# Optimization experiments

Measured on AMD Instinct MI355X. Metric: run time of the kernel, lower is better.

The kernel has to match this reference:

```python
import jax, jax.numpy as jnp
import numpy as np

B, S, D, H = 8, 1024, 1024, 16
DK = D // H


def setup_inputs() -> dict:
    key = jax.random.key(0)
    ks = jax.random.split(key, 10)
    scale = 1.0 / np.sqrt(D)
    return {
        "x": jax.random.normal(ks[0], (B, S, D), dtype=jnp.float32),
        "prefix": jax.random.randint(ks[1], (B,), 0, S, dtype=jnp.int32),
        "Wq": jax.random.normal(ks[2], (D, D), dtype=jnp.float32) * scale,
        "bq": jnp.zeros((D,), dtype=jnp.float32),
        "Wk": jax.random.normal(ks[3], (D, D), dtype=jnp.float32) * scale,
        "bk": jnp.zeros((D,), dtype=jnp.float32),
        "Wv": jax.random.normal(ks[4], (D, D), dtype=jnp.float32) * scale,
        "bv": jnp.zeros((D,), dtype=jnp.float32),
        "Wo": jax.random.normal(ks[5], (D, D), dtype=jnp.float32) * scale,
        "bo": jnp.zeros((D,), dtype=jnp.float32),
    }


def reference(x, prefix, Wq, bq, Wk, bk, Wv, bv, Wo, bo):
    b, s, d = x.shape
    h, dk = H, DK
    # projections -> [b, h, s, dk]
    def split_heads(t):
        return t.reshape(b, s, h, dk).transpose(0, 2, 1, 3)
    q = split_heads(x @ Wq + bq)
    k = split_heads(x @ Wk + bk)
    v = split_heads(x @ Wv + bv)
    # raw scores (no 1/sqrt(dk) scaling in the original)
    scores = jnp.einsum('bhqd,bhkd->bhqk', q, k)
    # mask construction (faithful to original, incl. final permute/transpose):
    # allowed[b, q, k] = (q < prefix[b]) or (k >= q)
    q_idx = jnp.arange(s)[:, None]   # [s, 1]
    k_idx = jnp.arange(s)[None, :]   # [1, s]
    allowed = (q_idx[None, :, :] < prefix[:, None, None]) | (k_idx >= q_idx)  # [b, s, s]
    scores = jnp.where(allowed[:, None, :, :], scores, -jnp.inf)
    probs = jax.nn.softmax(scores, axis=-1)
    # einsum -> bqhd, then transpose(1,2) -> bhqd, then view(b, s, d) (faithful
    # to the original's head-interleaving reshape)
    out = jnp.einsum('bhql,bhld->bqhd', probs, v)
    out = out.transpose(0, 2, 1, 3).reshape(b, s, d)
    return out @ Wo + bo
```

## Files before the change

### kernel.cpp

```cpp
#include <hip/hip_runtime.h>
#include <stdint.h>

typedef __attribute__((ext_vector_type(8)))  short          short8;
typedef __attribute__((ext_vector_type(8)))  unsigned short u16x8;
typedef __attribute__((ext_vector_type(4)))  unsigned short u16x4;
typedef __attribute__((ext_vector_type(4)))  float          f32x4;
typedef __attribute__((ext_vector_type(16))) float          f32x16;

__device__ __forceinline__ unsigned short f2bf(float x) {
  unsigned int u = __float_as_uint(x);
  u += 0x7fffu + ((u >> 16) & 1u);
  return (unsigned short)(u >> 16);
}
__device__ __forceinline__ float bf2f(unsigned short b) {
  return __uint_as_float(((unsigned int)b) << 16);
}

__device__ __forceinline__ void mfma16(f32x4& c, short8 a, short8 b) {
  asm volatile("v_mfma_f32_16x16x32_bf16 %0, %1, %2, %0" : "+v"(c) : "v"(a), "v"(b));
}
__device__ __forceinline__ void mfma32(f32x16& c, short8 a, short8 b) {
  asm volatile("v_mfma_f32_32x32x16_bf16 %0, %1, %2, %0" : "+v"(c) : "v"(a), "v"(b));
}
__device__ __forceinline__ float hw_exp2(float x) {
  float r;
  asm("v_exp_f32 %0, %1" : "=v"(r) : "v"(x));
  return r;
}

#define GLDS(gsrc, ldst)                                                    \
  __builtin_amdgcn_global_load_lds(                                         \
      (const __attribute__((address_space(1))) void*)(gsrc),                \
      (__attribute__((address_space(3))) void*)(ldst), 16, 0, 0)

__global__ void split_x_kernel(const float4* __restrict__ x,
                               ushort4* __restrict__ xh, int n4) {
  int stride = gridDim.x * blockDim.x;
  for (int i = blockIdx.x * blockDim.x + threadIdx.x; i < n4; i += stride) {
    float4 v = x[i];
    ushort4 h;
    h.x = f2bf(v.x);
    h.y = f2bf(v.y);
    h.z = f2bf(v.z);
    h.w = f2bf(v.w);
    xh[i] = h;
  }
}

__global__ void wsplit_kernel(const float* __restrict__ Wq, const float* __restrict__ Wk,
                              const float* __restrict__ Wv, const float* __restrict__ Wo,
                              unsigned short* qkv, unsigned short* oh) {
  __shared__ float tile[32][33];
  int z = blockIdx.z;
  const float* W = (z == 0) ? Wq : (z == 1) ? Wk : (z == 2) ? Wv : Wo;
  unsigned short* Oh = (z < 3) ? qkv + (size_t)z * 1024 * 1024 : oh;
  int k0 = blockIdx.y * 32, n0 = blockIdx.x * 32;
  int tx = threadIdx.x & 31, ty = threadIdx.x >> 5;
#pragma unroll
  for (int j = 0; j < 4; ++j)
    tile[ty + 8 * j][tx] = W[(size_t)(k0 + ty + 8 * j) * 1024 + n0 + tx];
  __syncthreads();
#pragma unroll
  for (int j = 0; j < 4; ++j) {
    float v = tile[tx][ty + 8 * j];
    size_t idx = (size_t)(n0 + ty + 8 * j) * 1024 + k0 + tx;
    Oh[idx] = f2bf(v);
  }
}

__global__ __launch_bounds__(256)
void qkv_gemm_kernel(const unsigned short* __restrict__ Ah,
                     const unsigned short* __restrict__ Bh,
                     const float* __restrict__ bq, const float* __restrict__ bk,
                     const float* __restrict__ bv,
                     unsigned short* __restrict__ QK, unsigned short* __restrict__ VT) {
  __shared__ unsigned short smem[128 * 136];
  unsigned short* sAh = smem;
  unsigned short* sBh = smem + 8192;
  const int K = 1024, M = 8192;

  int t = threadIdx.x;
  int wid = t >> 6, l = t & 63;
  int wm = wid >> 1, wn = wid & 1;
  int bm = blockIdx.y * 128, bn = blockIdx.x * 128;

  f32x4 acc[4][4] = {};

  for (int k0 = 0; k0 < K; k0 += 64) {
#pragma unroll
    for (int r = 0; r < 4; ++r) {
      int o = (r * 256 + t) << 4;
      int row = o >> 7;
      int gce = ((o & 127) ^ ((row & 7) << 4)) >> 1;
      int wb  = (o & ~1023) >> 1;
      size_t gA = (size_t)(bm + row) * K + k0 + gce;
      size_t gB = (size_t)(bn + row) * K + k0 + gce;
      GLDS(Ah + gA, sAh + wb);
      GLDS(Bh + gB, sBh + wb);
    }
    __syncthreads();
#pragma unroll
    for (int kh = 0; kh < 2; ++kh) {
      short8 afh[4], bfh[4];
#pragma unroll
      for (int m = 0; m < 4; ++m) {
        int row = wm * 64 + m * 16 + (l & 15);
        int cb = (((l >> 4) * 16 + kh * 64) ^ ((row & 7) << 4)) >> 1;
        afh[m] = *(const short8*)(sAh + row * 64 + cb);
      }
#pragma unroll
      for (int n = 0; n < 4; ++n) {
        int row = wn * 64 + n * 16 + (l & 15);
        int cb = (((l >> 4) * 16 + kh * 64) ^ ((row & 7) << 4)) >> 1;
        bfh[n] = *(const short8*)(sBh + row * 64 + cb);
      }
#pragma unroll
      for (int m = 0; m < 4; ++m)
#pragma unroll
        for (int n = 0; n < 4; ++n)
          mfma16(acc[m][n], afh[m], bfh[n]);
    }
    __syncthreads();
  }

  if (bn >= 2048) {
    int vb = bn - 2048;
    unsigned short* sT = smem;
#pragma unroll
    for (int m = 0; m < 4; ++m) {
      int lrow0 = wm * 64 + m * 16 + (l >> 4) * 4;
#pragma unroll
      for (int n = 0; n < 4; ++n) {
        int lcol = wn * 64 + n * 16 + (l & 15);
        float bs = bv[vb + lcol];
        u16x4 w;
#pragma unroll
        for (int r = 0; r < 4; ++r) w[r] = f2bf(acc[m][n][r] + bs);
        *(u16x4*)&sT[lcol * 136 + lrow0] = w;
      }
    }
    __syncthreads();
#pragma unroll
    for (int j = 0; j < 8; ++j) {
      int c = (t >> 4) + 16 * j;
      int r = (t & 15) * 8;
      *(u16x8*)(VT + (size_t)(vb + c) * M + bm + r) = *(const u16x8*)&sT[c * 136 + r];
    }
    return;
  }

#pragma unroll
  for (int m = 0; m < 4; ++m) {
    int grow0 = bm + wm * 64 + m * 16 + (l >> 4) * 4;
#pragma unroll
    for (int n = 0; n < 4; ++n) {
      int gcol = bn + wn * 64 + n * 16 + (l & 15);
      float bs = (gcol < 1024) ? bq[gcol] : bk[gcol - 1024];
#pragma unroll
      for (int r = 0; r < 4; ++r)
        QK[(size_t)(grow0 + r) * 2048 + gcol] = f2bf(acc[m][n][r] + bs);
    }
  }
}

__global__ __launch_bounds__(256)
void gemm_out_kernel(const unsigned short* __restrict__ Ah,
                     const unsigned short* __restrict__ Bh,
                     const float* __restrict__ bias, float* __restrict__ Cf,
                     int M, int N, int K) {
  __shared__ unsigned short smem[2 * 8192];
  unsigned short* sAh = smem;
  unsigned short* sBh = smem + 8192;

  int t = threadIdx.x;
  int wid = t >> 6, l = t & 63;
  int wm = wid >> 1, wn = wid & 1;
  int bm = blockIdx.y * 128, bn = blockIdx.x * 128;

  f32x4 acc[4][4] = {};

  for (int k0 = 0; k0 < K; k0 += 64) {
#pragma unroll
    for (int r = 0; r < 4; ++r) {
      int o = (r * 256 + t) << 4;
      int row = o >> 7;
      int gce = ((o & 127) ^ ((row & 7) << 4)) >> 1;
      int wb  = (o & ~1023) >> 1;
      size_t gA = (size_t)(bm + row) * K + k0 + gce;
      size_t gB = (size_t)(bn + row) * K + k0 + gce;
      GLDS(Ah + gA, sAh + wb);
      GLDS(Bh + gB, sBh + wb);
    }
    __syncthreads();
#pragma unroll
    for (int kh = 0; kh < 2; ++kh) {
      short8 afh[4], bfh[4];
#pragma unroll
      for (int m = 0; m < 4; ++m) {
        int row = wm * 64 + m * 16 + (l & 15);
        int cb = (((l >> 4) * 16 + kh * 64) ^ ((row & 7) << 4)) >> 1;
        afh[m] = *(const short8*)(sAh + row * 64 + cb);
      }
#pragma unroll
      for (int n = 0; n < 4; ++n) {
        int row = wn * 64 + n * 16 + (l & 15);
        int cb = (((l >> 4) * 16 + kh * 64) ^ ((row & 7) << 4)) >> 1;
        bfh[n] = *(const short8*)(sBh + row * 64 + cb);
      }
#pragma unroll
      for (int m = 0; m < 4; ++m)
#pragma unroll
        for (int n = 0; n < 4; ++n)
          mfma16(acc[m][n], afh[m], bfh[n]);
    }
    __syncthreads();
  }
#pragma unroll
  for (int m = 0; m < 4; ++m) {
    int grow0 = bm + wm * 64 + m * 16 + (l >> 4) * 4;
#pragma unroll
    for (int n = 0; n < 4; ++n) {
      int gcol = bn + wn * 64 + n * 16 + (l & 15);
      float bs = bias[gcol];
#pragma unroll
      for (int r = 0; r < 4; ++r)
        Cf[(size_t)(grow0 + r) * N + gcol] = acc[m][n][r] + bs;
    }
  }
}

__global__ __launch_bounds__(128)
void attn_kernel(const unsigned short* __restrict__ QK,
                 const unsigned short* __restrict__ VT, const int* __restrict__ prefix,
                 unsigned short* __restrict__ AOh) {
  const float NEG = -3.0e38f;
  const float L2E = 1.4426950408889634f;
  const float MC  = 46.16624410f;
  __shared__ unsigned short sKh[2][32][66];
  __shared__ unsigned short sV [2][64][34];

  int bh = blockIdx.x;
  int b = bh >> 4, h = bh & 15;
  int t = threadIdx.x, wid = t >> 6, l = t & 63;
  int qb0 = blockIdx.y * 64;
  int qb = qb0 + wid * 32;
  int P = prefix[b];
  int lq = l & 31, g = l >> 5;
  int q = qb + lq;
  bool qfull = (q < P);
  bool allfull = (P >= qb + 32);

  short8 bqh[4];
  {
    size_t base = (size_t)(b * 1024 + q) * 2048 + h * 64 + g * 8;
#pragma unroll
    for (int c = 0; c < 4; ++c)
      bqh[c] = *(const short8*)(QK + base + c * 16);
  }

  const unsigned short* KhB = QK + (size_t)b * 1024 * 2048 + 1024 + h * 64;
  const unsigned short* VTB = VT + (size_t)(h * 64) * 8192 + b * 1024;

  int srow = t >> 3, scol = (t & 7) * 8;
  int vrow = t >> 2, vcol = (t & 3) * 8;

  int kt0 = (qb0 >= P) ? qb0 : 0;
  int ntiles = (1024 - kt0) >> 5;

  f32x16 o0 = {}, o1 = {};
  float lrun = 0.f;

  int cur = 0;
  auto body = [&](int kt) {
    bool wave_dead = (qb >= P) && (kt + 31 < qb);
    if (wave_dead) return;
    f32x16 s = {};
    __builtin_amdgcn_s_setprio(1);
#pragma unroll
    for (int c = 0; c < 4; ++c) {
      short8 ah = *(const short8*)&sKh[cur][lq][g * 8 + c * 16];
      mfma32(s, ah, bqh[c]);
    }
    __builtin_amdgcn_s_setprio(0);

    float p[16];
    if (allfull || kt > qb) {
#pragma unroll
      for (int r = 0; r < 16; ++r)
        p[r] = hw_exp2(__builtin_fmaf(s[r], L2E, -MC));
    } else {
#pragma unroll
      for (int r = 0; r < 16; ++r) {
        int k = kt + (r & 3) + 8 * (r >> 2) + 4 * g;
        float sv = (qfull || k >= q) ? s[r] : NEG;
        p[r] = hw_exp2(__builtin_fmaf(sv, L2E, -MC));
      }
    }
    float s01 = p[0] + p[1],  s23 = p[2] + p[3],  s45 = p[4] + p[5],  s67 = p[6] + p[7];
    float s89 = p[8] + p[9],  sab = p[10] + p[11], scd = p[12] + p[13], sef = p[14] + p[15];
    lrun += ((s01 + s23) + (s45 + s67)) + ((s89 + sab) + (scd + sef));

    unsigned int w0, w1, w2, w3, w4, w5, w6, w7;
    asm("v_cvt_pk_bf16_f32 %0, %1, %2" : "=v"(w0) : "v"(p[0]),  "v"(p[1]));
    asm("v_cvt_pk_bf16_f32 %0, %1, %2" : "=v"(w1) : "v"(p[2]),  "v"(p[3]));
    asm("v_cvt_pk_bf16_f32 %0, %1, %2" : "=v"(w2) : "v"(p[4]),  "v"(p[5]));
    asm("v_cvt_pk_bf16_f32 %0, %1, %2" : "=v"(w3) : "v"(p[6]),  "v"(p[7]));
    asm("v_cvt_pk_bf16_f32 %0, %1, %2" : "=v"(w4) : "v"(p[8]),  "v"(p[9]));
    asm("v_cvt_pk_bf16_f32 %0, %1, %2" : "=v"(w5) : "v"(p[10]), "v"(p[11]));
    asm("v_cvt_pk_bf16_f32 %0, %1, %2" : "=v"(w6) : "v"(p[12]), "v"(p[13]));
    asm("v_cvt_pk_bf16_f32 %0, %1, %2" : "=v"(w7) : "v"(p[14]), "v"(p[15]));
    {
      unsigned int v0 = g ? w0 : w2, r0 = __shfl_xor(v0, 32);
      unsigned int v1 = g ? w1 : w3, r1 = __shfl_xor(v1, 32);
      unsigned int v4 = g ? w4 : w6, r4 = __shfl_xor(v4, 32);
      unsigned int v5 = g ? w5 : w7, r5 = __shfl_xor(v5, 32);
      unsigned int n0 = g ? r0 : w0, n2 = g ? w2 : r0;
      unsigned int n1 = g ? r1 : w1, n3 = g ? w3 : r1;
      unsigned int n4 = g ? r4 : w4, n6 = g ? w6 : r4;
      unsigned int n5 = g ? r5 : w5, n7 = g ? w7 : r5;
      w0 = n0; w1 = n1; w2 = n2; w3 = n3; w4 = n4; w5 = n5; w6 = n6; w7 = n7;
    }
    union { unsigned int u[4]; short8 v; } B0, B1;
    B0.u[0] = w0; B0.u[1] = w1; B0.u[2] = w2; B0.u[3] = w3;
    B1.u[0] = w4; B1.u[1] = w5; B1.u[2] = w6; B1.u[3] = w7;

    short8 va00 = *(const short8*)&sV[cur][lq][g * 8];
    short8 va01 = *(const short8*)&sV[cur][lq][16 + g * 8];
    short8 va10 = *(const short8*)&sV[cur][32 + lq][g * 8];
    short8 va11 = *(const short8*)&sV[cur][32 + lq][16 + g * 8];
    __builtin_amdgcn_s_setprio(1);
    mfma32(o0, va00, B0.v);
    mfma32(o0, va01, B1.v);
    mfma32(o1, va10, B0.v);
    mfma32(o1, va11, B1.v);
    __builtin_amdgcn_s_setprio(0);
  };

  u16x8 akh0, akh1, av0, av1;
  u16x8 bkh0, bkh1, bv0, bv1;
  akh0 = *(const u16x8*)(KhB + (size_t)(kt0 + srow) * 2048 + scol);
  akh1 = *(const u16x8*)(KhB + (size_t)(kt0 + srow + 16) * 2048 + scol);
  av0  = *(const u16x8*)(VTB + (size_t)vrow * 8192 + kt0 + vcol);
  av1  = *(const u16x8*)(VTB + (size_t)(vrow + 32) * 8192 + kt0 + vcol);
  *(u16x8*)&sKh[0][srow][scol]      = akh0;
  *(u16x8*)&sKh[0][srow + 16][scol] = akh1;
  *(u16x8*)&sV [0][vrow][vcol]      = av0;
  *(u16x8*)&sV [0][vrow + 32][vcol] = av1;
  {
    int kt1 = kt0 + ((1 < ntiles) ? 32 : 0);
    akh0 = *(const u16x8*)(KhB + (size_t)(kt1 + srow) * 2048 + scol);
    akh1 = *(const u16x8*)(KhB + (size_t)(kt1 + srow + 16) * 2048 + scol);
    av0  = *(const u16x8*)(VTB + (size_t)vrow * 8192 + kt1 + vcol);
    av1  = *(const u16x8*)(VTB + (size_t)(vrow + 32) * 8192 + kt1 + vcol);
  }
  __syncthreads();

  int i = 0;
  while (true) {
    {
      int i2 = (i + 2 < ntiles) ? (i + 2) : (ntiles - 1);
      int kt2 = kt0 + i2 * 32;
      bkh0 = *(const u16x8*)(KhB + (size_t)(kt2 + srow) * 2048 + scol);
      bkh1 = *(const u16x8*)(KhB + (size_t)(kt2 + srow + 16) * 2048 + scol);
      bv0  = *(const u16x8*)(VTB + (size_t)vrow * 8192 + kt2 + vcol);
      bv1  = *(const u16x8*)(VTB + (size_t)(vrow + 32) * 8192 + kt2 + vcol);
      body(kt0 + i * 32);
      if (i + 1 < ntiles) {
        *(u16x8*)&sKh[cur ^ 1][srow][scol]      = akh0;
        *(u16x8*)&sKh[cur ^ 1][srow + 16][scol] = akh1;
        *(u16x8*)&sV [cur ^ 1][vrow][vcol]      = av0;
        *(u16x8*)&sV [cur ^ 1][vrow + 32][vcol] = av1;
      }
      __syncthreads();
      cur ^= 1; ++i;
      if (i >= ntiles) break;
    }
    {
      int i2 = (i + 2 < ntiles) ? (i + 2) : (ntiles - 1);
      int kt2 = kt0 + i2 * 32;
      akh0 = *(const u16x8*)(KhB + (size_t)(kt2 + srow) * 2048 + scol);
      akh1 = *(const u16x8*)(KhB + (size_t)(kt2 + srow + 16) * 2048 + scol);
      av0  = *(const u16x8*)(VTB + (size_t)vrow * 8192 + kt2 + vcol);
      av1  = *(const u16x8*)(VTB + (size_t)(vrow + 32) * 8192 + kt2 + vcol);
      body(kt0 + i * 32);
      if (i + 1 < ntiles) {
        *(u16x8*)&sKh[cur ^ 1][srow][scol]      = bkh0;
        *(u16x8*)&sKh[cur ^ 1][srow + 16][scol] = bkh1;
        *(u16x8*)&sV [cur ^ 1][vrow][vcol]      = bv0;
        *(u16x8*)&sV [cur ^ 1][vrow + 32][vcol] = bv1;
      }
      __syncthreads();
      cur ^= 1; ++i;
      if (i >= ntiles) break;
    }
  }

  lrun += __shfl_xor(lrun, 32);

  float inv = 1.0f / lrun;
  size_t obase = (size_t)(b * 1024 + h * 64 + (q >> 4)) * 1024 + (q & 15) * 64;
#pragma unroll
  for (int tt = 0; tt < 4; ++tt) {
    u16x4 w0, w1;
#pragma unroll
    for (int j = 0; j < 4; ++j) {
      w0[j] = f2bf(o0[4 * tt + j] * inv);
      w1[j] = f2bf(o1[4 * tt + j] * inv);
    }
    *(u16x4*)(AOh + obase + 8 * tt + 4 * g)      = w0;
    *(u16x4*)(AOh + obase + 32 + 8 * tt + 4 * g) = w1;
  }
}

extern "C" void kernel_launch(void* const* d_in, const int* in_sizes, int n_in,
                              void* d_out, int out_size, void* d_ws, size_t ws_size,
                              hipStream_t stream) {
  (void)in_sizes; (void)n_in; (void)out_size;
  const float* x      = (const float*)d_in[0];
  const int*   prefix = (const int*)d_in[1];
  const float* Wq = (const float*)d_in[2];
  const float* bq = (const float*)d_in[3];
  const float* Wk = (const float*)d_in[4];
  const float* bk = (const float*)d_in[5];
  const float* Wv = (const float*)d_in[6];
  const float* bv = (const float*)d_in[7];
  const float* Wo = (const float*)d_in[8];
  const float* bo = (const float*)d_in[9];
  float* out = (float*)d_out;

  const size_t MBY = 1ull << 20;
  if (ws_size < 144 * MBY) return;
  char* ws = (char*)d_ws;
  unsigned short* xh   = (unsigned short*)(ws + 0 * MBY);
  unsigned short* wqkv = (unsigned short*)(ws + 32 * MBY);
  unsigned short* woh  = (unsigned short*)(ws + 44 * MBY);
  unsigned short* QK   = (unsigned short*)(ws + 48 * MBY);
  unsigned short* AOh  = (unsigned short*)(ws + 112 * MBY);
  unsigned short* VT   = (unsigned short*)(ws + 128 * MBY);

  split_x_kernel<<<1024, 256, 0, stream>>>((const float4*)x, (ushort4*)xh, 8192 * 1024 / 4);
  wsplit_kernel<<<dim3(32, 32, 4), 256, 0, stream>>>(Wq, Wk, Wv, Wo, wqkv, woh);
  qkv_gemm_kernel<<<dim3(24, 64), 256, 0, stream>>>(xh, wqkv, bq, bk, bv, QK, VT);
  attn_kernel<<<dim3(128, 16), 128, 0, stream>>>(QK, VT, prefix, AOh);
  gemm_out_kernel<<<dim3(8, 64), 256, 0, stream>>>(AOh, woh, bo, out, 8192, 1024, 1024);
}
```

Before: 166.5 us.

## Load attention K/V tiles directly into registers with single-wave blocks

The attention kernel drops the shared-memory K/V staging and its barriers. Each single-wave block now loads its K and V MFMA fragments straight from global memory into registers, double-buffered two tiles ahead, and the grid doubles to match. K/V tiles are no longer shared between two waves, so global/L2 traffic per query block roughly doubles. The per-wave dead-tile skip is also gone, so each block now starts directly at its own start tile.

```diff
diff --git a/kernel.cpp b/kernel.cpp
--- a/kernel.cpp
+++ b/kernel.cpp
@@ -11,9 +11,6 @@
   unsigned int u = __float_as_uint(x);
   u += 0x7fffu + ((u >> 16) & 1u);
   return (unsigned short)(u >> 16);
-}
-__device__ __forceinline__ float bf2f(unsigned short b) {
-  return __uint_as_float(((unsigned int)b) << 16);
 }
 
 __device__ __forceinline__ void mfma16(f32x4& c, short8 a, short8 b) {
@@ -229,23 +226,20 @@
   }
 }
 
-__global__ __launch_bounds__(128)
+__global__ __launch_bounds__(64)
 void attn_kernel(const unsigned short* __restrict__ QK,
                  const unsigned short* __restrict__ VT, const int* __restrict__ prefix,
                  unsigned short* __restrict__ AOh) {
   const float NEG = -3.0e38f;
   const float L2E = 1.4426950408889634f;
   const float MC  = 46.16624410f;
-  __shared__ unsigned short sKh[2][32][66];
-  __shared__ unsigned short sV [2][64][34];
 
   int bh = blockIdx.x;
   int b = bh >> 4, h = bh & 15;
-  int t = threadIdx.x, wid = t >> 6, l = t & 63;
-  int qb0 = blockIdx.y * 64;
-  int qb = qb0 + wid * 32;
+  int l = threadIdx.x;
+  int lq = l & 31, g = l >> 5;
+  int qb = blockIdx.y * 32;
   int P = prefix[b];
-  int lq = l & 31, g = l >> 5;
   int q = qb + lq;
   bool qfull = (q < P);
   bool allfull = (P >= qb + 32);
@@ -258,29 +252,34 @@
       bqh[c] = *(const short8*)(QK + base + c * 16);
   }
 
-  const unsigned short* KhB = QK + (size_t)b * 1024 * 2048 + 1024 + h * 64;
-  const unsigned short* VTB = VT + (size_t)(h * 64) * 8192 + b * 1024;
-
-  int srow = t >> 3, scol = (t & 7) * 8;
-  int vrow = t >> 2, vcol = (t & 3) * 8;
-
-  int kt0 = (qb0 >= P) ? qb0 : 0;
+  const unsigned short* KhB = QK + (size_t)b * 1024 * 2048 + 1024 + h * 64 + g * 8;
+  const unsigned short* VTB = VT + (size_t)(h * 64 + lq) * 8192 + b * 1024 + g * 8;
+
+  int kt0 = (qb >= P) ? qb : 0;
   int ntiles = (1024 - kt0) >> 5;
 
   f32x16 o0 = {}, o1 = {};
   float lrun = 0.f;
 
-  int cur = 0;
-  auto body = [&](int kt) {
-    bool wave_dead = (qb >= P) && (kt + 31 < qb);
-    if (wave_dead) return;
+  auto loadK = [&](int kt, short8* kf) {
+    size_t rb = (size_t)(kt + lq) * 2048;
+#pragma unroll
+    for (int c = 0; c < 4; ++c)
+      kf[c] = *(const short8*)(KhB + rb + c * 16);
+  };
+  auto loadV = [&](int kt, short8* vf) {
+    vf[0] = *(const short8*)(VTB + kt);
+    vf[1] = *(const short8*)(VTB + kt + 16);
+    vf[2] = *(const short8*)(VTB + (size_t)32 * 8192 + kt);
+    vf[3] = *(const short8*)(VTB + (size_t)32 * 8192 + kt + 16);
+  };
+
+  auto body = [&](int kt, const short8* kf, const short8* vf) {
     f32x16 s = {};
     __builtin_amdgcn_s_setprio(1);
 #pragma unroll
-    for (int c = 0; c < 4; ++c) {
-      short8 ah = *(const short8*)&sKh[cur][lq][g * 8 + c * 16];
-      mfma32(s, ah, bqh[c]);
-    }
+    for (int c = 0; c < 4; ++c)
+      mfma32(s, kf[c], bqh[c]);
     __builtin_amdgcn_s_setprio(0);
 
     float p[16];
@@ -324,74 +323,40 @@
     B0.u[0] = w0; B0.u[1] = w1; B0.u[2] = w2; B0.u[3] = w3;
     B1.u[0] = w4; B1.u[1] = w5; B1.u[2] = w6; B1.u[3] = w7;
 
-    short8 va00 = *(const short8*)&sV[cur][lq][g * 8];
-    short8 va01 = *(const short8*)&sV[cur][lq][16 + g * 8];
-    short8 va10 = *(const short8*)&sV[cur][32 + lq][g * 8];
-    short8 va11 = *(const short8*)&sV[cur][32 + lq][16 + g * 8];
     __builtin_amdgcn_s_setprio(1);
-    mfma32(o0, va00, B0.v);
-    mfma32(o0, va01, B1.v);
-    mfma32(o1, va10, B0.v);
-    mfma32(o1, va11, B1.v);
+    mfma32(o0, vf[0], B0.v);
+    mfma32(o0, vf[1], B1.v);
+    mfma32(o1, vf[2], B0.v);
+    mfma32(o1, vf[3], B1.v);
     __builtin_amdgcn_s_setprio(0);
   };
 
-  u16x8 akh0, akh1, av0, av1;
-  u16x8 bkh0, bkh1, bv0, bv1;
-  akh0 = *(const u16x8*)(KhB + (size_t)(kt0 + srow) * 2048 + scol);
-  akh1 = *(const u16x8*)(KhB + (size_t)(kt0 + srow + 16) * 2048 + scol);
-  av0  = *(const u16x8*)(VTB + (size_t)vrow * 8192 + kt0 + vcol);
-  av1  = *(const u16x8*)(VTB + (size_t)(vrow + 32) * 8192 + kt0 + vcol);
-  *(u16x8*)&sKh[0][srow][scol]      = akh0;
-  *(u16x8*)&sKh[0][srow + 16][scol] = akh1;
-  *(u16x8*)&sV [0][vrow][vcol]      = av0;
-  *(u16x8*)&sV [0][vrow + 32][vcol] = av1;
+  short8 kA[4], vA[4], kB[4], vB[4];
+  loadK(kt0, kA);
+  loadV(kt0, vA);
   {
-    int kt1 = kt0 + ((1 < ntiles) ? 32 : 0);
-    akh0 = *(const u16x8*)(KhB + (size_t)(kt1 + srow) * 2048 + scol);
-    akh1 = *(const u16x8*)(KhB + (size_t)(kt1 + srow + 16) * 2048 + scol);
-    av0  = *(const u16x8*)(VTB + (size_t)vrow * 8192 + kt1 + vcol);
-    av1  = *(const u16x8*)(VTB + (size_t)(vrow + 32) * 8192 + kt1 + vcol);
-  }
-  __syncthreads();
+    int kt1 = kt0 + ((ntiles > 1) ? 32 : 0);
+    loadK(kt1, kB);
+    loadV(kt1, vB);
+  }
 
   int i = 0;
   while (true) {
     {
-      int i2 = (i + 2 < ntiles) ? (i + 2) : (ntiles - 1);
-      int kt2 = kt0 + i2 * 32;
-      bkh0 = *(const u16x8*)(KhB + (size_t)(kt2 + srow) * 2048 + scol);
-      bkh1 = *(const u16x8*)(KhB + (size_t)(kt2 + srow + 16) * 2048 + scol);
-      bv0  = *(const u16x8*)(VTB + (size_t)vrow * 8192 + kt2 + vcol);
-      bv1  = *(const u16x8*)(VTB + (size_t)(vrow + 32) * 8192 + kt2 + vcol);
-      body(kt0 + i * 32);
-      if (i + 1 < ntiles) {
-        *(u16x8*)&sKh[cur ^ 1][srow][scol]      = akh0;
-        *(u16x8*)&sKh[cur ^ 1][srow + 16][scol] = akh1;
-        *(u16x8*)&sV [cur ^ 1][vrow][vcol]      = av0;
-        *(u16x8*)&sV [cur ^ 1][vrow + 32][vcol] = av1;
-      }
-      __syncthreads();
-      cur ^= 1; ++i;
-      if (i >= ntiles) break;
+      body(kt0 + i * 32, kA, vA);
+      if (i + 2 < ntiles) {
+        loadK(kt0 + (i + 2) * 32, kA);
+        loadV(kt0 + (i + 2) * 32, vA);
+      }
+      ++i; if (i >= ntiles) break;
     }
     {
-      int i2 = (i + 2 < ntiles) ? (i + 2) : (ntiles - 1);
-      int kt2 = kt0 + i2 * 32;
-      akh0 = *(const u16x8*)(KhB + (size_t)(kt2 + srow) * 2048 + scol);
-      akh1 = *(const u16x8*)(KhB + (size_t)(kt2 + srow + 16) * 2048 + scol);
-      av0  = *(const u16x8*)(VTB + (size_t)vrow * 8192 + kt2 + vcol);
-      av1  = *(const u16x8*)(VTB + (size_t)(vrow + 32) * 8192 + kt2 + vcol);
-      body(kt0 + i * 32);
-      if (i + 1 < ntiles) {
-        *(u16x8*)&sKh[cur ^ 1][srow][scol]      = bkh0;
-        *(u16x8*)&sKh[cur ^ 1][srow + 16][scol] = bkh1;
-        *(u16x8*)&sV [cur ^ 1][vrow][vcol]      = bv0;
-        *(u16x8*)&sV [cur ^ 1][vrow + 32][vcol] = bv1;
-      }
-      __syncthreads();
-      cur ^= 1; ++i;
-      if (i >= ntiles) break;
+      body(kt0 + i * 32, kB, vB);
+      if (i + 2 < ntiles) {
+        loadK(kt0 + (i + 2) * 32, kB);
+        loadV(kt0 + (i + 2) * 32, vB);
+      }
+      ++i; if (i >= ntiles) break;
     }
   }
 
@@ -441,6 +406,6 @@
   split_x_kernel<<<1024, 256, 0, stream>>>((const float4*)x, (ushort4*)xh, 8192 * 1024 / 4);
   wsplit_kernel<<<dim3(32, 32, 4), 256, 0, stream>>>(Wq, Wk, Wv, Wo, wqkv, woh);
   qkv_gemm_kernel<<<dim3(24, 64), 256, 0, stream>>>(xh, wqkv, bq, bk, bv, QK, VT);
-  attn_kernel<<<dim3(128, 16), 128, 0, stream>>>(QK, VT, prefix, AOh);
+  attn_kernel<<<dim3(128, 32), 64, 0, stream>>>(QK, VT, prefix, AOh);
   gemm_out_kernel<<<dim3(8, 64), 256, 0, stream>>>(AOh, woh, bo, out, 8192, 1024, 1024);
 }
```

Result: slower. 207.3 us (+24.5%).

## Software-pipeline QK^T with softmax/PV in attention and merge prep kernels

Applied to the files above, without the earlier changes.

The attention loop is restructured so the QK^T MFMAs for tile i are issued before the softmax and PV work of tile i-1. This overlaps matrix-core work with exp and conversion ALU work, at the cost of an extra barrier per iteration and another live score accumulator. Separately, the x-to-bf16 conversion and the weight transpose/convert kernels are merged into one launch to cut launch overhead. The extra barrier and register pressure could reduce the benefit.

```diff
diff --git a/kernel.cpp b/kernel.cpp
--- a/kernel.cpp
+++ b/kernel.cpp
@@ -12,9 +12,6 @@
   u += 0x7fffu + ((u >> 16) & 1u);
   return (unsigned short)(u >> 16);
 }
-__device__ __forceinline__ float bf2f(unsigned short b) {
-  return __uint_as_float(((unsigned int)b) << 16);
-}
 
 __device__ __forceinline__ void mfma16(f32x4& c, short8 a, short8 b) {
   asm volatile("v_mfma_f32_16x16x32_bf16 %0, %1, %2, %0" : "+v"(c) : "v"(a), "v"(b));
@@ -33,25 +30,22 @@
       (const __attribute__((address_space(1))) void*)(gsrc),                \
       (__attribute__((address_space(3))) void*)(ldst), 16, 0, 0)
 
-__global__ void split_x_kernel(const float4* __restrict__ x,
-                               ushort4* __restrict__ xh, int n4) {
-  int stride = gridDim.x * blockDim.x;
-  for (int i = blockIdx.x * blockDim.x + threadIdx.x; i < n4; i += stride) {
-    float4 v = x[i];
-    ushort4 h;
-    h.x = f2bf(v.x);
-    h.y = f2bf(v.y);
-    h.z = f2bf(v.z);
-    h.w = f2bf(v.w);
-    xh[i] = h;
-  }
-}
-
-__global__ void wsplit_kernel(const float* __restrict__ Wq, const float* __restrict__ Wk,
-                              const float* __restrict__ Wv, const float* __restrict__ Wo,
-                              unsigned short* qkv, unsigned short* oh) {
+__global__ void prep_kernel(const float4* __restrict__ x, ushort4* __restrict__ xh,
+                            const float* __restrict__ Wq, const float* __restrict__ Wk,
+                            const float* __restrict__ Wv, const float* __restrict__ Wo,
+                            unsigned short* qkv, unsigned short* oh) {
+  int z = blockIdx.z;
+  if (z == 4) {
+    int lb = blockIdx.y * 32 + blockIdx.x;
+    for (int i = lb * 256 + threadIdx.x; i < 2097152; i += 262144) {
+      float4 v = x[i];
+      ushort4 h;
+      h.x = f2bf(v.x); h.y = f2bf(v.y); h.z = f2bf(v.z); h.w = f2bf(v.w);
+      xh[i] = h;
+    }
+    return;
+  }
   __shared__ float tile[32][33];
-  int z = blockIdx.z;
   const float* W = (z == 0) ? Wq : (z == 1) ? Wk : (z == 2) ? Wv : Wo;
   unsigned short* Oh = (z < 3) ? qkv + (size_t)z * 1024 * 1024 : oh;
   int k0 = blockIdx.y * 32, n0 = blockIdx.x * 32;
@@ -270,19 +264,19 @@
   f32x16 o0 = {}, o1 = {};
   float lrun = 0.f;
 
-  int cur = 0;
-  auto body = [&](int kt) {
-    bool wave_dead = (qb >= P) && (kt + 31 < qb);
-    if (wave_dead) return;
-    f32x16 s = {};
+  auto qkt = [&](f32x16& s, int cb) {
+    s = f32x16{};
     __builtin_amdgcn_s_setprio(1);
 #pragma unroll
     for (int c = 0; c < 4; ++c) {
-      short8 ah = *(const short8*)&sKh[cur][lq][g * 8 + c * 16];
+      short8 ah = *(const short8*)&sKh[cb][lq][g * 8 + c * 16];
       mfma32(s, ah, bqh[c]);
     }
     __builtin_amdgcn_s_setprio(0);
-
+  };
+
+  auto finish = [&](int kt, const f32x16& s, int vb) {
+    if ((qb >= P) && (kt + 31 < qb)) return;
     float p[16];
     if (allfull || kt > qb) {
 #pragma unroll
@@ -324,10 +318,10 @@
     B0.u[0] = w0; B0.u[1] = w1; B0.u[2] = w2; B0.u[3] = w3;
     B1.u[0] = w4; B1.u[1] = w5; B1.u[2] = w6; B1.u[3] = w7;
 
-    short8 va00 = *(const short8*)&sV[cur][lq][g * 8];
-    short8 va01 = *(const short8*)&sV[cur][lq][16 + g * 8];
-    short8 va10 = *(const short8*)&sV[cur][32 + lq][g * 8];
-    short8 va11 = *(const short8*)&sV[cur][32 + lq][16 + g * 8];
+    short8 va00 = *(const short8*)&sV[vb][lq][g * 8];
+    short8 va01 = *(const short8*)&sV[vb][lq][16 + g * 8];
+    short8 va10 = *(const short8*)&sV[vb][32 + lq][g * 8];
+    short8 va11 = *(const short8*)&sV[vb][32 + lq][16 + g * 8];
     __builtin_amdgcn_s_setprio(1);
     mfma32(o0, va00, B0.v);
     mfma32(o0, va01, B1.v);
@@ -355,8 +349,26 @@
   }
   __syncthreads();
 
-  int i = 0;
-  while (true) {
+  f32x16 sA, sB;
+  qkt(sB, 0);
+  if (1 < ntiles) {
+    *(u16x8*)&sKh[1][srow][scol]      = akh0;
+    *(u16x8*)&sKh[1][srow + 16][scol] = akh1;
+    *(u16x8*)&sV [1][vrow][vcol]      = av0;
+    *(u16x8*)&sV [1][vrow + 32][vcol] = av1;
+  }
+  {
+    int i2 = (2 < ntiles) ? 2 : (ntiles - 1);
+    int kt2 = kt0 + i2 * 32;
+    akh0 = *(const u16x8*)(KhB + (size_t)(kt2 + srow) * 2048 + scol);
+    akh1 = *(const u16x8*)(KhB + (size_t)(kt2 + srow + 16) * 2048 + scol);
+    av0  = *(const u16x8*)(VTB + (size_t)vrow * 8192 + kt2 + vcol);
+    av1  = *(const u16x8*)(VTB + (size_t)(vrow + 32) * 8192 + kt2 + vcol);
+  }
+  __syncthreads();
+
+  int i = 1;
+  while (i < ntiles) {
     {
       int i2 = (i + 2 < ntiles) ? (i + 2) : (ntiles - 1);
       int kt2 = kt0 + i2 * 32;
@@ -364,16 +376,18 @@
       bkh1 = *(const u16x8*)(KhB + (size_t)(kt2 + srow + 16) * 2048 + scol);
       bv0  = *(const u16x8*)(VTB + (size_t)vrow * 8192 + kt2 + vcol);
       bv1  = *(const u16x8*)(VTB + (size_t)(vrow + 32) * 8192 + kt2 + vcol);
-      body(kt0 + i * 32);
+      int cb = i & 1;
+      qkt(sA, cb);
+      finish(kt0 + (i - 1) * 32, sB, cb ^ 1);
+      __syncthreads();
       if (i + 1 < ntiles) {
-        *(u16x8*)&sKh[cur ^ 1][srow][scol]      = akh0;
-        *(u16x8*)&sKh[cur ^ 1][srow + 16][scol] = akh1;
-        *(u16x8*)&sV [cur ^ 1][vrow][vcol]      = av0;
-        *(u16x8*)&sV [cur ^ 1][vrow + 32][vcol] = av1;
+        *(u16x8*)&sKh[cb ^ 1][srow][scol]      = akh0;
+        *(u16x8*)&sKh[cb ^ 1][srow + 16][scol] = akh1;
+        *(u16x8*)&sV [cb ^ 1][vrow][vcol]      = av0;
+        *(u16x8*)&sV [cb ^ 1][vrow + 32][vcol] = av1;
       }
       __syncthreads();
-      cur ^= 1; ++i;
-      if (i >= ntiles) break;
+      ++i; if (i >= ntiles) break;
     }
     {
       int i2 = (i + 2 < ntiles) ? (i + 2) : (ntiles - 1);
@@ -382,17 +396,24 @@
       akh1 = *(const u16x8*)(KhB + (size_t)(kt2 + srow + 16) * 2048 + scol);
       av0  = *(const u16x8*)(VTB + (size_t)vrow * 8192 + kt2 + vcol);
       av1  = *(const u16x8*)(VTB + (size_t)(vrow + 32) * 8192 + kt2 + vcol);
-      body(kt0 + i * 32);
+      int cb = i & 1;
+      qkt(sB, cb);
+      finish(kt0 + (i - 1) * 32, sA, cb ^ 1);
+      __syncthreads();
       if (i + 1 < ntiles) {
-        *(u16x8*)&sKh[cur ^ 1][srow][scol]      = bkh0;
-        *(u16x8*)&sKh[cur ^ 1][srow + 16][scol] = bkh1;
-        *(u16x8*)&sV [cur ^ 1][vrow][vcol]      = bv0;
-        *(u16x8*)&sV [cur ^ 1][vrow + 32][vcol] = bv1;
+        *(u16x8*)&sKh[cb ^ 1][srow][scol]      = bkh0;
+        *(u16x8*)&sKh[cb ^ 1][srow + 16][scol] = bkh1;
+        *(u16x8*)&sV [cb ^ 1][vrow][vcol]      = bv0;
+        *(u16x8*)&sV [cb ^ 1][vrow + 32][vcol] = bv1;
       }
       __syncthreads();
-      cur ^= 1; ++i;
-      if (i >= ntiles) break;
-    }
+      ++i; if (i >= ntiles) break;
+    }
+  }
+  {
+    int last = ntiles - 1;
+    if (last & 1) finish(kt0 + last * 32, sA, last & 1);
+    else          finish(kt0 + last * 32, sB, last & 1);
   }
 
   lrun += __shfl_xor(lrun, 32);
@@ -438,8 +459,8 @@
   unsigned short* AOh  = (unsigned short*)(ws + 112 * MBY);
   unsigned short* VT   = (unsigned short*)(ws + 128 * MBY);
 
-  split_x_kernel<<<1024, 256, 0, stream>>>((const float4*)x, (ushort4*)xh, 8192 * 1024 / 4);
-  wsplit_kernel<<<dim3(32, 32, 4), 256, 0, stream>>>(Wq, Wk, Wv, Wo, wqkv, woh);
+  prep_kernel<<<dim3(32, 32, 5), 256, 0, stream>>>((const float4*)x, (ushort4*)xh,
+                                                   Wq, Wk, Wv, Wo, wqkv, woh);
   qkv_gemm_kernel<<<dim3(24, 64), 256, 0, stream>>>(xh, wqkv, bq, bk, bv, QK, VT);
   attn_kernel<<<dim3(128, 16), 128, 0, stream>>>(QK, VT, prefix, AOh);
   gemm_out_kernel<<<dim3(8, 64), 256, 0, stream>>>(AOh, woh, bo, out, 8192, 1024, 1024);
```

After: 174.5 us. 4.8% more time.
